# Kernel tuning notes

Measured on AMD Instinct MI355X. Metric: run time of the kernel, lower is better.

## Reference

```python
import jax, jax.numpy as jnp
import numpy as np

C = 64            # multiplicity of 0e and 1o in in_irreps
N_NODES = 20000
N_EDGES = 320000
RAD_DIM = 8
HID = 64
NUM_IRREPS_OUT = 4 * C   # 2C x 0e + 2C x 1o -> 256 scalar weights
AVG_NUM_NEIGHBORS = 16.0


def setup_inputs() -> dict:
    key = jax.random.key(0)
    ks = jax.random.split(key, 10)
    node_feats = jax.random.normal(ks[0], (N_NODES, C + 3 * C), jnp.float32)
    vectors = jax.random.normal(ks[1], (N_EDGES, 3), jnp.float32)
    radial_embedding = jax.random.normal(ks[2], (N_EDGES, RAD_DIM), jnp.float32)
    senders = jax.random.randint(ks[3], (N_EDGES,), 0, N_NODES, jnp.int32)
    receivers = jax.random.randint(ks[4], (N_EDGES,), 0, N_NODES, jnp.int32)
    # e3nn-style MLP params (no bias), forward scales by 1/sqrt(fan_in)
    W0 = jax.random.normal(ks[5], (RAD_DIM, HID), jnp.float32)
    W1 = jax.random.normal(ks[6], (HID, HID), jnp.float32)
    W2 = jax.random.normal(ks[7], (HID, HID), jnp.float32)
    W3 = jax.random.normal(ks[8], (HID, NUM_IRREPS_OUT), jnp.float32)
    return {"node_feats": node_feats, "vectors": vectors,
            "radial_embedding": radial_embedding, "senders": senders,
            "receivers": receivers, "W0": W0, "W1": W1, "W2": W2, "W3": W3}


def _mlp(x, W0, W1, W2, W3):
    # MultiLayerPerceptron with gradient_normalization=1.0: scale by 1/sqrt(fan_in)
    h = jax.nn.silu(x @ W0 / jnp.sqrt(jnp.asarray(W0.shape[0], x.dtype)))
    h = jax.nn.silu(h @ W1 / jnp.sqrt(jnp.asarray(HID, x.dtype)))
    h = jax.nn.silu(h @ W2 / jnp.sqrt(jnp.asarray(HID, x.dtype)))
    return h @ W3 / jnp.sqrt(jnp.asarray(HID, x.dtype))


def reference(node_feats, vectors, radial_embedding, senders, receivers, W0, W1, W2, W3):
    n = node_feats.shape[0]
    s = node_feats[:, :C]                      # [N, C]  0e block
    v = node_feats[:, C:].reshape(n, C, 3)     # [N, C, 3]  1o block
    s_e = s[senders]                           # gather  [E, C]
    v_e = v[senders]                           # gather  [E, C, 3]
    # spherical harmonics l=1 of -vectors, normalized input, component norm
    r = -vectors
    Y = jnp.sqrt(3.0) * r / jnp.linalg.norm(r, axis=-1, keepdims=True)  # [E, 3]
    # CG tensor product filtered to target irreps (0e + 1o):
    tp_v = s_e[:, :, None] * Y[:, None, :]                 # 0e x 1o -> 1o  [E,C,3]
    tp_s = jnp.einsum('eci,ei->ec', v_e, Y) / jnp.sqrt(3.0)  # 1o x 1o -> 0e  [E,C]
    msg_s = jnp.concatenate([s_e, tp_s], axis=-1)          # [E, 2C]
    msg_v = jnp.concatenate([v_e, tp_v], axis=1)           # [E, 2C, 3]
    # per-irrep MLP gate from radial embedding
    mix = _mlp(radial_embedding, W0, W1, W2, W3)           # [E, 4C]
    msg_s = msg_s * mix[:, :2 * C]
    msg_v = msg_v * mix[:, 2 * C:, None]
    # scatter-add into receivers
    out_s = jnp.zeros((n, 2 * C), msg_s.dtype).at[receivers].add(msg_s)
    out_v = jnp.zeros((n, 2 * C, 3), msg_v.dtype).at[receivers].add(msg_v)
    out = jnp.concatenate([out_s, out_v.reshape(n, 6 * C)], axis=-1)
    return out / AVG_NUM_NEIGHBORS                         # [N, 512]
```

## Files before the change

kernel.cpp:

```cpp
#include <hip/hip_runtime.h>

typedef __attribute__((ext_vector_type(8))) short bf16x8;
typedef __attribute__((ext_vector_type(4))) float f32x4;

static __device__ __forceinline__ unsigned short f2bf(float f) {
    unsigned int u = __float_as_uint(f);
    unsigned int r = (u + 0x7fffu + ((u >> 16) & 1u)) >> 16;
    return (unsigned short)r;
}
static __device__ __forceinline__ float bf2f(unsigned short h) {
    return __uint_as_float(((unsigned int)h) << 16);
}

#define WP_TOTAL 26624

__global__ __launch_bounds__(256) void prep_kernel(
    const float* __restrict__ W0, const float* __restrict__ W1,
    const float* __restrict__ W2, const float* __restrict__ W3,
    unsigned short* __restrict__ Wp,
    const int* __restrict__ recv, int* __restrict__ cnt, int E)
{
    int o = blockIdx.x * 256 + threadIdx.x;
    if (o < WP_TOTAL) {
        float val;
        if (o < 2048) {
            int nt = o >> 9, w = o & 511, lane = w >> 3, j = w & 7;
            int k = (lane >> 4) * 8 + j, n = nt * 16 + (lane & 15);
            val = (k < 8) ? W0[k * 64 + n] * 0.35355339059327373f : 0.f;
        } else if (o < 6144) {
            int oo = o - 2048, fid = oo >> 9, w = oo & 511, lane = w >> 3, j = w & 7;
            int nt = fid >> 1, ks = fid & 1;
            int k = ks * 32 + (lane >> 4) * 8 + j, n = nt * 16 + (lane & 15);
            val = W1[k * 64 + n] * 0.125f;
        } else if (o < 10240) {
            int oo = o - 6144, fid = oo >> 9, w = oo & 511, lane = w >> 3, j = w & 7;
            int nt = fid >> 1, ks = fid & 1;
            int k = ks * 32 + (lane >> 4) * 8 + j, n = nt * 16 + (lane & 15);
            val = W2[k * 64 + n] * 0.125f;
        } else {
            int oo = o - 10240, fid = oo >> 9, w = oo & 511, lane = w >> 3, j = w & 7;
            int nt = fid >> 1, ks = fid & 1;
            int k = ks * 32 + (lane >> 4) * 8 + j, n = nt * 16 + (lane & 15);
            val = W3[k * 256 + n] * 0.125f;
        }
        Wp[o] = f2bf(val);
    }
    if (o < E) atomicAdd(&cnt[recv[o]], 1);
}

__global__ __launch_bounds__(1024) void scan_kernel(const int* __restrict__ cnt,
                                                    int* __restrict__ off,
                                                    int* __restrict__ cursor, int N)
{
    __shared__ int part[1024];
    int t = threadIdx.x;
    int per = (N + 1023) / 1024;
    int base = t * per;
    int s = 0;
    for (int i = 0; i < per; ++i) { int idx = base + i; if (idx < N) s += cnt[idx]; }
    part[t] = s;
    __syncthreads();
    for (int d = 1; d < 1024; d <<= 1) {
        int v = (t >= d) ? part[t - d] : 0;
        __syncthreads();
        part[t] += v;
        __syncthreads();
    }
    int run = (t == 0) ? 0 : part[t - 1];
    for (int i = 0; i < per; ++i) {
        int idx = base + i;
        if (idx < N) { off[idx] = run; cursor[idx] = run; run += cnt[idx]; }
    }
    if (t == 1023) off[N] = part[1023];
}

__global__ __launch_bounds__(256) void fill_kernel(
    const int*   __restrict__ recv,
    const int*   __restrict__ senders,
    const float* __restrict__ vectors,
    int* __restrict__ cursor,
    int* __restrict__ edge_of,
    int* __restrict__ snd_pos,
    float4* __restrict__ Y4,
    int E)
{
    int i = blockIdx.x * 256 + threadIdx.x;
    if (i < E) {
        int p = atomicAdd(&cursor[recv[i]], 1);
        edge_of[p] = i;
        snd_pos[p] = senders[i];
        float r0 = -vectors[(size_t)i * 3 + 0];
        float r1 = -vectors[(size_t)i * 3 + 1];
        float r2 = -vectors[(size_t)i * 3 + 2];
        float inv = rsqrtf(r0 * r0 + r1 * r1 + r2 * r2);
        const float s3 = 1.7320508075688772f;
        Y4[p] = make_float4(s3 * r0 * inv, s3 * r1 * inv, s3 * r2 * inv, 0.f);
    }
}

__global__ __launch_bounds__(256) void mlp_pos_kernel(
    const float* __restrict__ radial,
    const int* __restrict__ edge_of,
    const unsigned short* __restrict__ Wp,
    unsigned short* __restrict__ mix,
    int E)
{
    __shared__ __align__(16) unsigned short sW[10240];
    __shared__ __align__(16) unsigned short sH[4][1024];
    __shared__ __align__(16) unsigned short sM[4][16 * 68];

    const int t = threadIdx.x;
    {
        int4* dst = (int4*)sW;
        const int4* src = (const int4*)Wp;
        #pragma unroll
        for (int i = 0; i < 5; ++i) dst[t + i * 256] = src[t + i * 256];
    }
    __syncthreads();

    const int wv = t >> 6, l = t & 63;
    const int lrow = l & 15, quad = l >> 4;
    const int p0 = blockIdx.x * 64 + wv * 16;
    if (p0 >= E) return;

    unsigned short* H = sH[wv];
    unsigned short* M = sM[wv];

    bf16x8 afr = {0, 0, 0, 0, 0, 0, 0, 0};
    if (quad == 0) {
        int i = p0 + lrow; if (i >= E) i = E - 1;
        int e = edge_of[i];
        const float* rr = radial + (size_t)e * 8;
        float4 ra = *(const float4*)rr;
        float4 rb = *(const float4*)(rr + 4);
        afr[0] = (short)f2bf(ra.x); afr[1] = (short)f2bf(ra.y);
        afr[2] = (short)f2bf(ra.z); afr[3] = (short)f2bf(ra.w);
        afr[4] = (short)f2bf(rb.x); afr[5] = (short)f2bf(rb.y);
        afr[6] = (short)f2bf(rb.z); afr[7] = (short)f2bf(rb.w);
    }
    #pragma unroll
    for (int nt = 0; nt < 4; ++nt) {
        bf16x8 b = *(const bf16x8*)(sW + nt * 512 + l * 8);
        f32x4 z = {0.f, 0.f, 0.f, 0.f};
        f32x4 cf = __builtin_amdgcn_mfma_f32_16x16x32_bf16(afr, b, z, 0, 0, 0);
        #pragma unroll
        for (int r = 0; r < 4; ++r) {
            float v = cf[r];
            float h = v / (1.f + __expf(-v));
            int er = quad * 4 + r;
            int f  = nt * 16 + lrow;
            H[er * 64 + (f ^ ((er & 7) << 3))] = f2bf(h);
        }
    }

    #pragma unroll 1
    for (int L = 0; L < 2; ++L) {
        const unsigned short* WL = sW + 2048 + L * 4096;
        bf16x8 a[2];
        #pragma unroll
        for (int ks = 0; ks < 2; ++ks)
            a[ks] = *(const bf16x8*)(H + lrow * 64 + ((ks * 32 + quad * 8) ^ ((lrow & 7) << 3)));
        f32x4 cf[4];
        #pragma unroll
        for (int nt = 0; nt < 4; ++nt) { f32x4 z = {0.f,0.f,0.f,0.f}; cf[nt] = z; }
        #pragma unroll
        for (int ks = 0; ks < 2; ++ks) {
            #pragma unroll
            for (int nt = 0; nt < 4; ++nt) {
                bf16x8 b = *(const bf16x8*)(WL + (nt * 2 + ks) * 512 + l * 8);
                cf[nt] = __builtin_amdgcn_mfma_f32_16x16x32_bf16(a[ks], b, cf[nt], 0, 0, 0);
            }
        }
        #pragma unroll
        for (int nt = 0; nt < 4; ++nt) {
            #pragma unroll
            for (int r = 0; r < 4; ++r) {
                float v = cf[nt][r];
                float h = v / (1.f + __expf(-v));
                int er = quad * 4 + r;
                int f  = nt * 16 + lrow;
                H[er * 64 + (f ^ ((er & 7) << 3))] = f2bf(h);
            }
        }
    }

    bf16x8 a3[2];
    #pragma unroll
    for (int ks = 0; ks < 2; ++ks)
        a3[ks] = *(const bf16x8*)(H + lrow * 64 + ((ks * 32 + quad * 8) ^ ((lrow & 7) << 3)));

    const unsigned short* W3 = Wp + 10240;
    #pragma unroll 1
    for (int g = 0; g < 4; ++g) {
        f32x4 cf[4];
        #pragma unroll
        for (int np = 0; np < 4; ++np) { f32x4 z = {0.f,0.f,0.f,0.f}; cf[np] = z; }
        #pragma unroll
        for (int ks = 0; ks < 2; ++ks) {
            #pragma unroll
            for (int np = 0; np < 4; ++np) {
                int nt = g * 4 + np;
                bf16x8 b = *(const bf16x8*)(W3 + (nt * 2 + ks) * 512 + l * 8);
                cf[np] = __builtin_amdgcn_mfma_f32_16x16x32_bf16(a3[ks], b, cf[np], 0, 0, 0);
            }
        }
        #pragma unroll
        for (int np = 0; np < 4; ++np) {
            int c2 = np * 16 + lrow;
            #pragma unroll
            for (int r = 0; r < 4; ++r)
                M[(quad * 4 + r) * 68 + c2] = f2bf(cf[np][r]);
        }
        #pragma unroll
        for (int i = 0; i < 4; ++i) {
            int ri = i * 4 + quad;
            ushort4 v = *(const ushort4*)&M[ri * 68 + lrow * 4];
            if (p0 + ri < E)
                *(ushort4*)&mix[(size_t)(p0 + ri) * 256 + g * 64 + lrow * 4] = v;
        }
    }
}

__global__ __launch_bounds__(256) void gather_kernel(
    const float* __restrict__ node_feats,
    const int*   __restrict__ snd_pos,
    const float4* __restrict__ Y4,
    const int*   __restrict__ off,
    const unsigned short* __restrict__ mix,
    float* __restrict__ out, int N)
{
    int wid  = threadIdx.x >> 6;
    int lane = threadIdx.x & 63;
    int n = blockIdx.x * 4 + wid;
    if (n >= N) return;

    int beg = off[n], end = off[n + 1];

    float a0 = 0.f, a1 = 0.f;
    float b0 = 0.f, b1 = 0.f, b2 = 0.f;
    float c0 = 0.f, c1 = 0.f, c2 = 0.f;

    const float is3 = 0.5773502691896258f;

    #pragma unroll 4
    for (int i = beg; i < end; ++i) {
        int snd  = snd_pos[i];
        float4 Y = Y4[i];

        const float* nf = node_feats + (size_t)snd * 256;
        float s_e = nf[lane];
        float v0  = nf[64 + lane * 3 + 0];
        float v1  = nf[64 + lane * 3 + 1];
        float v2  = nf[64 + lane * 3 + 2];

        const unsigned short* m = mix + (size_t)i * 256;
        float m0 = bf2f(m[lane]);
        float m1 = bf2f(m[64 + lane]);
        float m2 = bf2f(m[128 + lane]);
        float m3 = bf2f(m[192 + lane]);

        float tp_s = (v0 * Y.x + v1 * Y.y + v2 * Y.z) * is3;

        a0 += s_e * m0;
        a1 += tp_s * m1;
        b0 += v0 * m2; b1 += v1 * m2; b2 += v2 * m2;
        float sm = s_e * m3;
        c0 += Y.x * sm; c1 += Y.y * sm; c2 += Y.z * sm;
    }

    float* o = out + (size_t)n * 512;
    const float kk = 0.0625f;
    o[lane]      = a0 * kk;
    o[64 + lane] = a1 * kk;
    o[128 + lane * 3 + 0] = b0 * kk;
    o[128 + lane * 3 + 1] = b1 * kk;
    o[128 + lane * 3 + 2] = b2 * kk;
    o[320 + lane * 3 + 0] = c0 * kk;
    o[320 + lane * 3 + 1] = c1 * kk;
    o[320 + lane * 3 + 2] = c2 * kk;
}

#define HID 64
__global__ __launch_bounds__(256) void mlp_kernel(
    const float* __restrict__ radial,
    const float* __restrict__ W0g, const float* __restrict__ W1g,
    const float* __restrict__ W2g, const float* __restrict__ W3g,
    unsigned short* __restrict__ mix, int e1)
{
    __shared__ float  sHf[HID * 256];
    __shared__ float4 sW4[1024];

    const int t = threadIdx.x;
    const int e = blockIdx.x * 256 + t;
    const bool valid = e < e1;

    if (t < 128) sW4[t] = ((const float4*)W0g)[t];
    __syncthreads();

    float x[8];
    if (valid) {
        float4 ra = ((const float4*)radial)[(size_t)e * 2 + 0];
        float4 rb = ((const float4*)radial)[(size_t)e * 2 + 1];
        x[0]=ra.x; x[1]=ra.y; x[2]=ra.z; x[3]=ra.w;
        x[4]=rb.x; x[5]=rb.y; x[6]=rb.z; x[7]=rb.w;
    } else {
        #pragma unroll
        for (int k = 0; k < 8; ++k) x[k] = 0.f;
    }

    float acc[64];
    #pragma unroll
    for (int j = 0; j < 64; ++j) acc[j] = 0.f;
    #pragma unroll
    for (int k = 0; k < 8; ++k) {
        #pragma unroll
        for (int jq = 0; jq < 16; ++jq) {
            float4 w = sW4[k * 16 + jq];
            acc[jq*4+0] = fmaf(x[k], w.x, acc[jq*4+0]);
            acc[jq*4+1] = fmaf(x[k], w.y, acc[jq*4+1]);
            acc[jq*4+2] = fmaf(x[k], w.z, acc[jq*4+2]);
            acc[jq*4+3] = fmaf(x[k], w.w, acc[jq*4+3]);
        }
    }
    #pragma unroll
    for (int j = 0; j < 64; ++j) {
        float v = acc[j] * 0.35355339059327373f;
        sHf[j * 256 + t] = v / (1.f + __expf(-v));
    }
    __syncthreads();
    #pragma unroll
    for (int i = 0; i < 4; ++i) sW4[t + i * 256] = ((const float4*)W1g)[t + i * 256];
    __syncthreads();

    #pragma unroll
    for (int j = 0; j < 64; ++j) acc[j] = 0.f;
    #pragma unroll 2
    for (int k = 0; k < 64; ++k) {
        float hk = sHf[k * 256 + t];
        #pragma unroll
        for (int jq = 0; jq < 16; ++jq) {
            float4 w = sW4[k * 16 + jq];
            acc[jq*4+0] = fmaf(hk, w.x, acc[jq*4+0]);
            acc[jq*4+1] = fmaf(hk, w.y, acc[jq*4+1]);
            acc[jq*4+2] = fmaf(hk, w.z, acc[jq*4+2]);
            acc[jq*4+3] = fmaf(hk, w.w, acc[jq*4+3]);
        }
    }
    __syncthreads();
    #pragma unroll
    for (int i = 0; i < 4; ++i) sW4[t + i * 256] = ((const float4*)W2g)[t + i * 256];
    #pragma unroll
    for (int j = 0; j < 64; ++j) {
        float v = acc[j] * 0.125f;
        sHf[j * 256 + t] = v / (1.f + __expf(-v));
    }
    __syncthreads();

    #pragma unroll
    for (int j = 0; j < 64; ++j) acc[j] = 0.f;
    #pragma unroll 2
    for (int k = 0; k < 64; ++k) {
        float hk = sHf[k * 256 + t];
        #pragma unroll
        for (int jq = 0; jq < 16; ++jq) {
            float4 w = sW4[k * 16 + jq];
            acc[jq*4+0] = fmaf(hk, w.x, acc[jq*4+0]);
            acc[jq*4+1] = fmaf(hk, w.y, acc[jq*4+1]);
            acc[jq*4+2] = fmaf(hk, w.z, acc[jq*4+2]);
            acc[jq*4+3] = fmaf(hk, w.w, acc[jq*4+3]);
        }
    }
    __syncthreads();
    #pragma unroll
    for (int j = 0; j < 64; ++j) {
        float v = acc[j] * 0.125f;
        sHf[j * 256 + t] = v / (1.f + __expf(-v));
    }

    unsigned short* mrow = mix + (size_t)e * 256;
    #pragma unroll 1
    for (int jt = 0; jt < 4; ++jt) {
        #pragma unroll
        for (int i = 0; i < 4; ++i) {
            int m = t + i * 256;
            sW4[m] = ((const float4*)W3g)[(m >> 4) * 64 + jt * 16 + (m & 15)];
        }
        __syncthreads();

        #pragma unroll
        for (int j = 0; j < 64; ++j) acc[j] = 0.f;
        #pragma unroll 2
        for (int k = 0; k < 64; ++k) {
            float hk = sHf[k * 256 + t];
            #pragma unroll
            for (int jq = 0; jq < 16; ++jq) {
                float4 w = sW4[k * 16 + jq];
                acc[jq*4+0] = fmaf(hk, w.x, acc[jq*4+0]);
                acc[jq*4+1] = fmaf(hk, w.y, acc[jq*4+1]);
                acc[jq*4+2] = fmaf(hk, w.z, acc[jq*4+2]);
                acc[jq*4+3] = fmaf(hk, w.w, acc[jq*4+3]);
            }
        }
        if (valid) {
            #pragma unroll
            for (int j4 = 0; j4 < 16; ++j4) {
                ushort4 u;
                u.x = f2bf(acc[j4*4+0] * 0.125f);
                u.y = f2bf(acc[j4*4+1] * 0.125f);
                u.z = f2bf(acc[j4*4+2] * 0.125f);
                u.w = f2bf(acc[j4*4+3] * 0.125f);
                *reinterpret_cast<ushort4*>(&mrow[jt * 64 + j4 * 4]) = u;
            }
        }
        __syncthreads();
    }
}

__global__ __launch_bounds__(256) void scatter_kernel(
    const float* __restrict__ node_feats,
    const float* __restrict__ vectors,
    const int*   __restrict__ senders,
    const int*   __restrict__ receivers,
    const unsigned short* __restrict__ mix,
    float* __restrict__ out, int e0, int e1)
{
    int wid  = threadIdx.x >> 6;
    int lane = threadIdx.x & 63;
    int e = e0 + blockIdx.x * 4 + wid;
    if (e >= e1) return;

    int snd = senders[e];
    int rcv = receivers[e];

    float r0 = -vectors[(size_t)e * 3 + 0];
    float r1 = -vectors[(size_t)e * 3 + 1];
    float r2 = -vectors[(size_t)e * 3 + 2];
    float inv = rsqrtf(r0 * r0 + r1 * r1 + r2 * r2);
    float Y0 = 1.7320508075688772f * r0 * inv;
    float Y1 = 1.7320508075688772f * r1 * inv;
    float Y2 = 1.7320508075688772f * r2 * inv;

    const float* nf = node_feats + (size_t)snd * 256;
    float s_e = nf[lane];
    float v0 = nf[64 + lane * 3 + 0];
    float v1 = nf[64 + lane * 3 + 1];
    float v2 = nf[64 + lane * 3 + 2];

    float tp_s = (v0 * Y0 + v1 * Y1 + v2 * Y2) * 0.5773502691896258f;

    const unsigned short* m = mix + (size_t)(e - e0) * 256;
    float m0 = bf2f(m[lane]), m1 = bf2f(m[64 + lane]);
    float m2 = bf2f(m[128 + lane]), m3 = bf2f(m[192 + lane]);

    float* orow = out + (size_t)rcv * 512;
    const float kk = 0.0625f;
    atomicAdd(&orow[lane],      s_e  * m0 * kk);
    atomicAdd(&orow[64 + lane], tp_s * m1 * kk);
    float mv = m2 * kk;
    atomicAdd(&orow[128 + lane * 3 + 0], v0 * mv);
    atomicAdd(&orow[128 + lane * 3 + 1], v1 * mv);
    atomicAdd(&orow[128 + lane * 3 + 2], v2 * mv);
    float ms = s_e * m3 * kk;
    atomicAdd(&orow[320 + lane * 3 + 0], Y0 * ms);
    atomicAdd(&orow[320 + lane * 3 + 1], Y1 * ms);
    atomicAdd(&orow[320 + lane * 3 + 2], Y2 * ms);
}

extern "C" void kernel_launch(void* const* d_in, const int* in_sizes, int n_in,
                              void* d_out, int out_size, void* d_ws, size_t ws_size,
                              hipStream_t stream)
{
    const float* node_feats = (const float*)d_in[0];
    const float* vectors    = (const float*)d_in[1];
    const float* radial     = (const float*)d_in[2];
    const int*   senders    = (const int*)d_in[3];
    const int*   receivers  = (const int*)d_in[4];
    const float* W0         = (const float*)d_in[5];
    const float* W1         = (const float*)d_in[6];
    const float* W2         = (const float*)d_in[7];
    const float* W3         = (const float*)d_in[8];
    float* out = (float*)d_out;

    const int E = in_sizes[3];
    const int N = in_sizes[0] / 256;

    size_t mix_bytes = (size_t)E * 256 * sizeof(unsigned short);
    size_t mix_al    = (mix_bytes + 255) & ~(size_t)255;
    size_t int_bytes = (size_t)(N + (N + 1) + N + E + E) * sizeof(int);
    size_t int_al    = (int_bytes + 255) & ~(size_t)255;
    size_t y4_bytes  = (size_t)E * sizeof(float4);
    size_t y4_al     = (y4_bytes + 255) & ~(size_t)255;
    size_t wp_bytes  = (size_t)WP_TOTAL * sizeof(unsigned short);
    size_t need      = mix_al + int_al + y4_al + wp_bytes;

    if (ws_size >= need) {
        unsigned short* mix = (unsigned short*)d_ws;
        int* cnt      = (int*)((char*)d_ws + mix_al);
        int* off      = cnt + N;
        int* cursor   = off + (N + 1);
        int* edge_of  = cursor + N;
        int* snd_pos  = edge_of + E;
        float4* Y4    = (float4*)((char*)d_ws + mix_al + int_al);
        unsigned short* Wp = (unsigned short*)((char*)d_ws + mix_al + int_al + y4_al);

        hipMemsetAsync(cnt, 0, (size_t)N * sizeof(int), stream);

        prep_kernel<<<dim3((E + 255) / 256), dim3(256), 0, stream>>>(
            W0, W1, W2, W3, Wp, receivers, cnt, E);
        scan_kernel<<<dim3(1), dim3(1024), 0, stream>>>(cnt, off, cursor, N);
        fill_kernel<<<dim3((E + 255) / 256), dim3(256), 0, stream>>>(
            receivers, senders, vectors, cursor, edge_of, snd_pos, Y4, E);

        mlp_pos_kernel<<<dim3((E + 63) / 64), dim3(256), 0, stream>>>(
            radial, edge_of, Wp, mix, E);

        gather_kernel<<<dim3((N + 3) / 4), dim3(256), 0, stream>>>(
            node_feats, snd_pos, Y4, off, mix, out, N);
    } else {
        hipMemsetAsync(d_out, 0, (size_t)out_size * sizeof(float), stream);
        size_t per_edge = 256 * sizeof(unsigned short);
        long long chunk_ll = (long long)(ws_size / per_edge);
        int chunk = (chunk_ll > E) ? E : (int)chunk_ll;
        chunk &= ~255;
        if (chunk <= 0) chunk = 256;
        unsigned short* mix = (unsigned short*)d_ws;
        for (int s = 0; s < E; s += chunk) {
            int eend = s + chunk; if (eend > E) eend = E;
            int ne = eend - s;
            mlp_kernel<<<dim3((ne + 255) / 256), dim3(256), 0, stream>>>(
                radial + (size_t)s * 8, W0, W1, W2, W3, mix, ne);
            scatter_kernel<<<dim3((ne + 3) / 4), dim3(256), 0, stream>>>(
                node_feats, vectors, senders, receivers, mix, out, s, eend);
        }
    }
}
```

Before: 221.3 us.

## Chunk MLP and gather over node ranges and use wave-shuffle scan

Splits the MLP-gate and gather passes into four node-range chunks, so each chunk's mix buffer is consumed by the gather soon after it is written, while it may still sit in cache. The scan kernel's shared-memory Hillis-Steele loop is replaced by a wave-level shuffle scan plus a 16-entry cross-wave pass, removing many block barriers. In exchange there are more kernel launches. Each MLP launch still uses the full-E grid, and the surplus blocks read the offsets and exit early, which adds launch and scheduling overhead.

```diff
diff --git a/kernel.cpp b/kernel.cpp
--- a/kernel.cpp
+++ b/kernel.cpp
@@ -52,26 +52,32 @@
                                                     int* __restrict__ off,
                                                     int* __restrict__ cursor, int N)
 {
-    __shared__ int part[1024];
-    int t = threadIdx.x;
-    int per = (N + 1023) / 1024;
-    int base = t * per;
+    __shared__ int wsum[16];
+    const int t = threadIdx.x, lane = t & 63, wv = t >> 6;
+    const int per = (N + 1023) / 1024;
+    const int base = t * per;
     int s = 0;
     for (int i = 0; i < per; ++i) { int idx = base + i; if (idx < N) s += cnt[idx]; }
-    part[t] = s;
-    __syncthreads();
-    for (int d = 1; d < 1024; d <<= 1) {
-        int v = (t >= d) ? part[t - d] : 0;
-        __syncthreads();
-        part[t] += v;
-        __syncthreads();
-    }
-    int run = (t == 0) ? 0 : part[t - 1];
+    int inc = s;
+    #pragma unroll
+    for (int d = 1; d < 64; d <<= 1) {
+        int v = __shfl_up(inc, d, 64);
+        if (lane >= d) inc += v;
+    }
+    if (lane == 63) wsum[wv] = inc;
+    __syncthreads();
+    if (t == 0) {
+        int run = 0;
+        #pragma unroll
+        for (int w = 0; w < 16; ++w) { int v = wsum[w]; wsum[w] = run; run += v; }
+    }
+    __syncthreads();
+    int run = wsum[wv] + inc - s;
     for (int i = 0; i < per; ++i) {
         int idx = base + i;
         if (idx < N) { off[idx] = run; cursor[idx] = run; run += cnt[idx]; }
     }
-    if (t == 1023) off[N] = part[1023];
+    if (t == 1023) off[N] = wsum[15] + inc;
 }
 
 __global__ __launch_bounds__(256) void fill_kernel(
@@ -103,8 +109,12 @@
     const int* __restrict__ edge_of,
     const unsigned short* __restrict__ Wp,
     unsigned short* __restrict__ mix,
-    int E)
-{
+    const int* __restrict__ off, int n0, int n1)
+{
+    const int p_begin = off[n0];
+    const int p_end   = off[n1];
+    if (p_begin + blockIdx.x * 64 >= p_end) return;
+
     __shared__ __align__(16) unsigned short sW[10240];
     __shared__ __align__(16) unsigned short sH[4][1024];
     __shared__ __align__(16) unsigned short sM[4][16 * 68];
@@ -120,15 +130,15 @@
 
     const int wv = t >> 6, l = t & 63;
     const int lrow = l & 15, quad = l >> 4;
-    const int p0 = blockIdx.x * 64 + wv * 16;
-    if (p0 >= E) return;
+    const int p0 = p_begin + blockIdx.x * 64 + wv * 16;
+    if (p0 >= p_end) return;
 
     unsigned short* H = sH[wv];
     unsigned short* M = sM[wv];
 
     bf16x8 afr = {0, 0, 0, 0, 0, 0, 0, 0};
     if (quad == 0) {
-        int i = p0 + lrow; if (i >= E) i = E - 1;
+        int i = p0 + lrow; if (i >= p_end) i = p_end - 1;
         int e = edge_of[i];
         const float* rr = radial + (size_t)e * 8;
         float4 ra = *(const float4*)rr;
@@ -215,7 +225,7 @@
         for (int i = 0; i < 4; ++i) {
             int ri = i * 4 + quad;
             ushort4 v = *(const ushort4*)&M[ri * 68 + lrow * 4];
-            if (p0 + ri < E)
+            if (p0 + ri < p_end)
                 *(ushort4*)&mix[(size_t)(p0 + ri) * 256 + g * 64 + lrow * 4] = v;
         }
     }
@@ -227,12 +237,12 @@
     const float4* __restrict__ Y4,
     const int*   __restrict__ off,
     const unsigned short* __restrict__ mix,
-    float* __restrict__ out, int N)
+    float* __restrict__ out, int n0, int n1)
 {
     int wid  = threadIdx.x >> 6;
     int lane = threadIdx.x & 63;
-    int n = blockIdx.x * 4 + wid;
-    if (n >= N) return;
+    int n = n0 + blockIdx.x * 4 + wid;
+    if (n >= n1) return;
 
     int beg = off[n], end = off[n + 1];
 
@@ -511,11 +521,16 @@
         fill_kernel<<<dim3((E + 255) / 256), dim3(256), 0, stream>>>(
             receivers, senders, vectors, cursor, edge_of, snd_pos, Y4, E);
 
-        mlp_pos_kernel<<<dim3((E + 63) / 64), dim3(256), 0, stream>>>(
-            radial, edge_of, Wp, mix, E);
-
-        gather_kernel<<<dim3((N + 3) / 4), dim3(256), 0, stream>>>(
-            node_feats, snd_pos, Y4, off, mix, out, N);
+        const int NC = 4;
+        for (int c = 0; c < NC; ++c) {
+            int n0 = (int)((long long)N * c / NC);
+            int n1 = (int)((long long)N * (c + 1) / NC);
+            if (n0 >= n1) continue;
+            mlp_pos_kernel<<<dim3((E + 63) / 64), dim3(256), 0, stream>>>(
+                radial, edge_of, Wp, mix, off, n0, n1);
+            gather_kernel<<<dim3((n1 - n0 + 3) / 4), dim3(256), 0, stream>>>(
+                node_feats, snd_pos, Y4, off, mix, out, n0, n1);
+        }
     } else {
         hipMemsetAsync(d_out, 0, (size_t)out_size * sizeof(float), stream);
         size_t per_edge = 256 * sizeof(unsigned short);
```

New measurement: 271.4 us. +22.6%, slower.
